# Optimization experiments

Hardware: AMD Instinct MI355X
Metric: run time of the kernel (lower is better)

Reference implementation:

```python
import jax, jax.numpy as jnp
import numpy as np

# ---- config constants (SmolLM2Config defaults) ----
N_EMBD = 576
N_HEAD = 9
N_KV = 3
HEAD_DIM = N_EMBD // N_HEAD        # 64
DR = 8                              # low-rank RoPE dim per head
GQA = N_HEAD // N_KV                # 9 // 3 = 3
BLOCK = 4096
ROPE_THETA = 100000.0
GROUP = 64                          # quant group size
RESID = 32                          # residual (full-precision) length
KBITS = 2
VBITS = 2
CLIP = 10000.0
B, S = 2, 2064


def _rope_tables():
    # pre_compute_rope with r=4 frequency indexing -> tables of width 2*r = 8 == DR
    pos = np.arange(BLOCK).astype(np.float32)
    thetas = 1.0 / ROPE_THETA ** (np.arange(0, HEAD_DIM, 2).astype(np.float32) / HEAD_DIM)
    pt = np.outer(pos, thetas)                       # [BLOCK, 32]
    pt = np.concatenate([pt, pt], axis=-1)           # [BLOCK, 64]
    cos, sin = np.cos(pt), np.sin(pt)
    r = 4
    idxs = sorted(sum([[2 * int(k * HEAD_DIM / (2 * r)), 2 * int(k * HEAD_DIM / (2 * r)) + 1]
                       for k in range(r)], []))      # [0,1,16,17,32,33,48,49]
    return jnp.asarray(cos[:, idxs]), jnp.asarray(sin[:, idxs])

COS, SIN = _rope_tables()  # each [BLOCK, DR]


def apply_rope(x):
    # x: [b, h, s, DR]; rotate-half RoPE on the DR low-rank dims
    s = x.shape[2]
    half = DR // 2
    x1, x2 = x[..., :half], x[..., half:]
    rotated = jnp.concatenate([-x2, x1], axis=-1)
    return x * COS[:s, :] + rotated * SIN[:s, :]


def _fake_quant(x, mn, mx, bits):
    levels = 2.0 ** bits - 1.0
    scale = (mx - mn) / levels
    scale = jnp.where(scale == 0, 1.0, scale)
    q = jnp.round((x - mn) / scale)
    return q * scale + mn


def quant_key(k):
    # AsymGroupedQuantizerByChannel: per-channel asym 2-bit over groups of GROUP tokens (STE)
    b, h, s, d = k.shape
    kf = jnp.clip(k, -CLIP, CLIP).reshape(b * h * (s // GROUP), GROUP, d)
    mn = kf.min(axis=1, keepdims=True)
    mx = kf.max(axis=1, keepdims=True)
    deq = _fake_quant(kf, mn, mx, KBITS)
    out = kf + jax.lax.stop_gradient(deq - kf)  # straight-through estimator
    return out.reshape(b, h, s, d)


def quant_value(v):
    # AsymGroupedQuantizer: per-token asym 2-bit over channel groups of size GROUP (== head_dim)
    b, h, s, d = v.shape
    vc = jnp.clip(v, -CLIP, CLIP)
    vg = vc.reshape(b, h, s, d // GROUP, GROUP)
    mn = vg.min(axis=-1, keepdims=True)
    mx = vg.max(axis=-1, keepdims=True)
    deq = _fake_quant(vg, mn, mx, VBITS).reshape(b, h, s, d)
    return vc + jax.lax.stop_gradient(deq - vc)


def maybe_quantize_kv(k, v):
    # KIVI: quantize all but the residual window
    s = k.shape[2]
    key_quant_len = (s // RESID) * RESID     # 2048 for S=2064
    value_quant_len = max(0, s - RESID)      # 2032
    k = jnp.concatenate([quant_key(k[:, :, :key_quant_len]), k[:, :, key_quant_len:]], axis=2)
    v = jnp.concatenate([quant_value(v[:, :, :value_quant_len]), v[:, :, value_quant_len:]], axis=2)
    return k, v


def setup_inputs() -> dict:
    key = jax.random.key(0)
    ks = jax.random.split(key, 7)
    std = 0.02
    return {
        "x": jax.random.normal(ks[0], (B, S, N_EMBD), jnp.float32),
        "q_w": jax.random.normal(ks[1], (N_HEAD * (HEAD_DIM - DR), N_EMBD), jnp.float32) * std,
        "k_w": jax.random.normal(ks[2], (N_KV * (HEAD_DIM - DR), N_EMBD), jnp.float32) * std,
        "v_w": jax.random.normal(ks[3], (N_KV * HEAD_DIM, N_EMBD), jnp.float32) * std,
        "qr_w": jax.random.normal(ks[4], (N_HEAD * DR, N_EMBD), jnp.float32) * std,
        "kr_w": jax.random.normal(ks[5], (N_KV * DR, N_EMBD), jnp.float32) * std,
        "o_w": jax.random.normal(ks[6], (N_EMBD, N_EMBD), jnp.float32) * std,
    }


def reference(x, q_w, k_w, v_w, qr_w, kr_w, o_w):
    b, s, _ = x.shape
    # projections (Linear: x @ W^T), split heads, [b, h, s, d]
    q = (x @ q_w.T).reshape(b, s, N_HEAD, HEAD_DIM - DR).transpose(0, 2, 1, 3)
    k = (x @ k_w.T).reshape(b, s, N_KV, HEAD_DIM - DR).transpose(0, 2, 1, 3)
    v = (x @ v_w.T).reshape(b, s, N_KV, HEAD_DIM).transpose(0, 2, 1, 3)
    qr = apply_rope((x @ qr_w.T).reshape(b, s, N_HEAD, DR).transpose(0, 2, 1, 3))
    kr = apply_rope((x @ kr_w.T).reshape(b, s, N_KV, DR).transpose(0, 2, 1, 3))
    q = jnp.concatenate([q, qr], axis=-1)   # [b, 9, s, 64]
    k = jnp.concatenate([k, kr], axis=-1)   # [b, 3, s, 64]
    # KIVI 2-bit fake-quantization of KV (residual window kept full precision)
    k, v = maybe_quantize_kv(k, v)
    # GQA: expand kv heads to query heads
    k = jnp.repeat(k, GQA, axis=1)
    v = jnp.repeat(v, GQA, axis=1)
    # causal attention
    scale = 1.0 / jnp.sqrt(jnp.float32(HEAD_DIM))
    scores = jnp.einsum('bhqd,bhkd->bhqk', q, k) * scale
    mask = jnp.tril(jnp.ones((s, s), bool))
    scores = jnp.where(mask, scores, -jnp.inf)
    attn = jax.nn.softmax(scores, axis=-1)
    out = jnp.einsum('bhqk,bhkd->bhqd', attn, v)
    out = out.transpose(0, 2, 1, 3).reshape(b, s, N_EMBD)
    return out @ o_w.T
```

## Files before the change

kernel.cpp:

```cpp
#include <hip/hip_runtime.h>
#include <math.h>

#define S_LEN 2064
#define S_PAD 2112
#define NB 2
#define NH 9
#define NKV 3
#define HD 64
#define EMB 576
#define NTOK (NB*S_LEN)
#define LSTR 68
#define KSTR 72

#define QSZ (NB*NH*S_LEN*HD)
#define KSZ (NB*NKV*S_LEN*HD)
#define VSZ (NB*NKV*S_LEN*HD)
#define ASZ (NB*S_LEN*EMB)
#define KPK (NB*NKV*S_PAD*HD)

#define NSLOT_BH 85
#define NSLOTS (NB*NH*NSLOT_BH)

typedef float  f32x4  __attribute__((ext_vector_type(4)));
typedef short  s16x8  __attribute__((ext_vector_type(8)));

static __device__ __forceinline__ ushort f2bf(float x) {
  union { float f; unsigned u; } a; a.f = x;
  unsigned r = a.u + 0x7fffu + ((a.u >> 16) & 1u);
  return (ushort)(r >> 16);
}
static __device__ __forceinline__ float bf2f(ushort h) {
  union { unsigned u; float f; } a; a.u = ((unsigned)h) << 16;
  return a.f;
}
static __device__ __forceinline__ int cum8(int qt) {
  int a = qt >> 3, b = qt & 7;
  return (a + 1) * (4 * a + b);
}

__global__ __launch_bounds__(256)
void proj_kernel(const float* __restrict__ x,
                 const float* __restrict__ qw, const float* __restrict__ kw,
                 const float* __restrict__ vw, const float* __restrict__ qrw,
                 const float* __restrict__ krw,
                 float* __restrict__ Qb, float* __restrict__ Kb,
                 float* __restrict__ Vb) {
  __shared__ __align__(16) ushort Xhi[64*KSTR];
  __shared__ __align__(16) ushort Xlo[64*KSTR];
  __shared__ __align__(16) ushort Whi[64*KSTR];
  __shared__ __align__(16) ushort Wlo[64*KSTR];

  const int tid  = threadIdx.x;
  const int wave = tid >> 6;
  const int lane = tid & 63;
  const int g    = lane >> 4;
  const int c    = lane & 15;

  const int m0 = blockIdx.x * 64;
  const int n0 = blockIdx.y * 64;

  const int srow = tid >> 2;
  const int sseg = (tid & 3) * 16;
  int gm = m0 + srow; if (gm > NTOK-1) gm = NTOK-1;
  const float* xrow = x + (size_t)gm * EMB;
  const int col = n0 + srow;
  const float* wrow;
  if (col < 504)      wrow = qw  + (size_t)col       * EMB;
  else if (col < 672) wrow = kw  + (size_t)(col-504) * EMB;
  else if (col < 864) wrow = vw  + (size_t)(col-672) * EMB;
  else if (col < 936) wrow = qrw + (size_t)(col-864) * EMB;
  else                wrow = krw + (size_t)(col-936) * EMB;

  f32x4 acc[4];
  #pragma unroll
  for (int n=0;n<4;++n) acc[n] = (f32x4){0.f,0.f,0.f,0.f};

  for (int kc0 = 0; kc0 < EMB; kc0 += 64) {
    __syncthreads();
    {
      float xv[16], wv[16];
      #pragma unroll
      for (int i=0;i<4;++i) {
        float4 x4 = *(const float4*)(xrow + kc0 + sseg + 4*i);
        float4 w4 = *(const float4*)(wrow + kc0 + sseg + 4*i);
        xv[4*i+0]=x4.x; xv[4*i+1]=x4.y; xv[4*i+2]=x4.z; xv[4*i+3]=x4.w;
        wv[4*i+0]=w4.x; wv[4*i+1]=w4.y; wv[4*i+2]=w4.z; wv[4*i+3]=w4.w;
      }
      uint xh[8], xl[8], wh[8], wl[8];
      #pragma unroll
      for (int m=0;m<8;++m) {
        ushort h0 = f2bf(xv[2*m]),   h1 = f2bf(xv[2*m+1]);
        ushort l0 = f2bf(xv[2*m]   - bf2f(h0));
        ushort l1 = f2bf(xv[2*m+1] - bf2f(h1));
        xh[m] = (uint)h0 | ((uint)h1 << 16);
        xl[m] = (uint)l0 | ((uint)l1 << 16);
        ushort g0 = f2bf(wv[2*m]),   g1 = f2bf(wv[2*m+1]);
        ushort k0 = f2bf(wv[2*m]   - bf2f(g0));
        ushort k1 = f2bf(wv[2*m+1] - bf2f(g1));
        wh[m] = (uint)g0 | ((uint)g1 << 16);
        wl[m] = (uint)k0 | ((uint)k1 << 16);
      }
      const int lo = srow*KSTR + sseg;
      *(uint4*)&Xhi[lo]     = make_uint4(xh[0],xh[1],xh[2],xh[3]);
      *(uint4*)&Xhi[lo + 8] = make_uint4(xh[4],xh[5],xh[6],xh[7]);
      *(uint4*)&Xlo[lo]     = make_uint4(xl[0],xl[1],xl[2],xl[3]);
      *(uint4*)&Xlo[lo + 8] = make_uint4(xl[4],xl[5],xl[6],xl[7]);
      *(uint4*)&Whi[lo]     = make_uint4(wh[0],wh[1],wh[2],wh[3]);
      *(uint4*)&Whi[lo + 8] = make_uint4(wh[4],wh[5],wh[6],wh[7]);
      *(uint4*)&Wlo[lo]     = make_uint4(wl[0],wl[1],wl[2],wl[3]);
      *(uint4*)&Wlo[lo + 8] = make_uint4(wl[4],wl[5],wl[6],wl[7]);
    }
    __syncthreads();

    #pragma unroll
    for (int kc=0; kc<2; ++kc) {
      const int d = kc*32 + g*8;
      s16x8 x_h = *(const s16x8*)&Xhi[(16*wave + c)*KSTR + d];
      s16x8 x_l = *(const s16x8*)&Xlo[(16*wave + c)*KSTR + d];
      #pragma unroll
      for (int n=0;n<4;++n) {
        s16x8 w_h = *(const s16x8*)&Whi[(16*n + c)*KSTR + d];
        s16x8 w_l = *(const s16x8*)&Wlo[(16*n + c)*KSTR + d];
        acc[n] = __builtin_amdgcn_mfma_f32_16x16x32_bf16(x_h, w_h, acc[n], 0, 0, 0);
        acc[n] = __builtin_amdgcn_mfma_f32_16x16x32_bf16(x_l, w_h, acc[n], 0, 0, 0);
        acc[n] = __builtin_amdgcn_mfma_f32_16x16x32_bf16(x_h, w_l, acc[n], 0, 0, 0);
        acc[n] = __builtin_amdgcn_mfma_f32_16x16x32_bf16(x_l, w_l, acc[n], 0, 0, 0);
      }
    }
  }

  #pragma unroll
  for (int r=0;r<4;++r) {
    const int row = m0 + 16*wave + 4*g + r;
    if (row >= NTOK) continue;
    const int b = row / S_LEN, s = row % S_LEN;
    #pragma unroll
    for (int n=0;n<4;++n) {
      const int cc = n0 + 16*n + c;
      const float v = acc[n][r];
      if (cc < 504) {
        int h = cc / 56, d = cc % 56;
        Qb[(((size_t)(b*NH+h))*S_LEN + s)*HD + d] = v;
      } else if (cc < 672) {
        int h = (cc-504)/56, d = (cc-504)%56;
        Kb[(((size_t)(b*NKV+h))*S_LEN + s)*HD + d] = v;
      } else if (cc < 864) {
        int h = (cc-672)/64, d = (cc-672)%64;
        Vb[(((size_t)(b*NKV+h))*S_LEN + s)*HD + d] = v;
      } else if (cc < 936) {
        int h = (cc-864)/8, d = 56 + (cc-864)%8;
        Qb[(((size_t)(b*NH+h))*S_LEN + s)*HD + d] = v;
      } else {
        int h = (cc-936)/8, d = 56 + (cc-936)%8;
        Kb[(((size_t)(b*NKV+h))*S_LEN + s)*HD + d] = v;
      }
    }
  }
}

__global__ void rope_kernel(float* __restrict__ Qb, float* __restrict__ Kb) {
  const int idx = blockIdx.x * blockDim.x + threadIdx.x;
  const int total = NB*(NH+NKV)*S_LEN;
  if (idx >= total) return;
  const int s  = idx % S_LEN;
  const int bh = idx / S_LEN;
  const int b  = bh / (NH+NKV), hh = bh % (NH+NKV);
  float* base;
  if (hh < NH) base = Qb + (((size_t)(b*NH + hh))*S_LEN + s)*HD + 56;
  else         base = Kb + (((size_t)(b*NKV + (hh-NH)))*S_LEN + s)*HD + 56;

  float4 a = *(const float4*)(base);
  float4 c = *(const float4*)(base + 4);
  float xv[8] = {a.x,a.y,a.z,a.w,c.x,c.y,c.z,c.w};
  const float es[4] = {0.0f, 2.0f/64.0f, 32.0f/64.0f, 34.0f/64.0f};
  const float ps = (float)s;
  float o[8];
  #pragma unroll
  for (int j=0;j<4;++j) {
    float th  = 1.0f / powf(100000.0f, es[j]);
    float ang = ps * th;
    float cs = cosf(ang), sn = sinf(ang);
    o[j]   = xv[j]*cs   - xv[j+4]*sn;
    o[j+4] = xv[j+4]*cs + xv[j]*sn;
  }
  *(float4*)(base)     = make_float4(o[0],o[1],o[2],o[3]);
  *(float4*)(base + 4) = make_float4(o[4],o[5],o[6],o[7]);
}

__global__ void quant_key_kernel(float* __restrict__ Kb) {
  const int wid  = (blockIdx.x * blockDim.x + threadIdx.x) >> 6;
  const int lane = threadIdx.x & 63;
  if (wid >= NB*NKV*32) return;
  const int bkh = wid >> 5, sg = wid & 31;
  float* base = Kb + ((size_t)bkh*S_LEN + sg*64)*HD + lane;
  float vals[64];
  float mn = 1e30f, mx = -1e30f;
  #pragma unroll
  for (int s=0;s<64;++s) {
    float v = fminf(fmaxf(base[s*HD], -10000.0f), 10000.0f);
    vals[s] = v;
    mn = fminf(mn, v); mx = fmaxf(mx, v);
  }
  float scale = (mx - mn) / 3.0f;
  if (scale == 0.0f) scale = 1.0f;
  #pragma unroll
  for (int s=0;s<64;++s) {
    float q = rintf((vals[s] - mn) / scale);
    base[s*HD] = q * scale + mn;
  }
}

__global__ void quant_value_kernel(float* __restrict__ Vb) {
  const int wid  = (blockIdx.x * blockDim.x + threadIdx.x) >> 6;
  const int lane = threadIdx.x & 63;
  const int total = NB*NKV*2032;
  if (wid >= total) return;
  const int bkh = wid / 2032, s = wid % 2032;
  float* p = Vb + ((size_t)bkh*S_LEN + s)*HD + lane;
  float v = fminf(fmaxf(*p, -10000.0f), 10000.0f);
  float mn = v, mx = v;
  #pragma unroll
  for (int m=1;m<64;m<<=1) {
    mn = fminf(mn, __shfl_xor(mn, m));
    mx = fmaxf(mx, __shfl_xor(mx, m));
  }
  float scale = (mx - mn) / 3.0f;
  if (scale == 0.0f) scale = 1.0f;
  float q = rintf((v - mn) / scale);
  *p = q * scale + mn;
}

__global__ __launch_bounds__(256)
void pack_k_kernel(const float* __restrict__ Kb,
                   ushort* __restrict__ KhiG, ushort* __restrict__ KloG) {
  const int idx = blockIdx.x * blockDim.x + threadIdx.x;
  const int total = NB*NKV*S_PAD*8;
  if (idx >= total) return;
  const int bkv = idx / (S_PAD*8);
  const int rem = idx % (S_PAD*8);
  const int s = rem >> 3, d0 = (rem & 7) * 8;
  uint u_h[4], u_l[4];
  if (s < S_LEN) {
    const float* src = Kb + ((size_t)bkv*S_LEN + s)*HD + d0;
    float4 a = *(const float4*)(src);
    float4 b = *(const float4*)(src + 4);
    float v[8] = {a.x,a.y,a.z,a.w,b.x,b.y,b.z,b.w};
    ushort hb[8], lb[8];
    #pragma unroll
    for (int e=0;e<8;++e) {
      hb[e] = f2bf(v[e]);
      lb[e] = f2bf(v[e] - bf2f(hb[e]));
    }
    #pragma unroll
    for (int m=0;m<4;++m) {
      u_h[m] = (uint)hb[2*m] | ((uint)hb[2*m+1] << 16);
      u_l[m] = (uint)lb[2*m] | ((uint)lb[2*m+1] << 16);
    }
  } else {
    #pragma unroll
    for (int m=0;m<4;++m) { u_h[m] = 0; u_l[m] = 0; }
  }
  const size_t off = ((size_t)bkv*S_PAD + s)*HD + d0;
  *(uint4*)(KhiG + off) = make_uint4(u_h[0],u_h[1],u_h[2],u_h[3]);
  *(uint4*)(KloG + off) = make_uint4(u_l[0],u_l[1],u_l[2],u_l[3]);
}

__global__ __launch_bounds__(256)
void pack_v_kernel(const float* __restrict__ Vb,
                   ushort* __restrict__ VhiT) {
  __shared__ float T[64*LSTR];
  const int tid = threadIdx.x;
  const int bkv = blockIdx.x / 33;
  const int kt  = blockIdx.x % 33;
  const int kbase = kt * 64;

  {
    const int key = tid >> 2, c16 = (tid & 3) * 16;
    const int s = kbase + key;
    if (s < S_LEN) {
      const float* src = Vb + ((size_t)bkv*S_LEN + s)*HD + c16;
      #pragma unroll
      for (int i=0;i<4;++i) {
        float4 v = *(const float4*)(src + 4*i);
        *(float4*)(T + key*LSTR + c16 + 4*i) = v;
      }
    } else {
      #pragma unroll
      for (int i=0;i<4;++i)
        *(float4*)(T + key*LSTR + c16 + 4*i) = make_float4(0.f,0.f,0.f,0.f);
    }
  }
  __syncthreads();
  {
    const int d = tid >> 2, seg = tid & 3;
    ushort hb[16];
    #pragma unroll
    for (int kk=0;kk<16;++kk)
      hb[kk] = f2bf(T[(seg*16 + kk)*LSTR + d]);
    uint uh[8];
    #pragma unroll
    for (int m=0;m<8;++m)
      uh[m] = (uint)hb[2*m] | ((uint)hb[2*m+1] << 16);
    const size_t off = ((size_t)bkv*HD + d)*S_PAD + kbase + seg*16;
    *(uint4*)(VhiT + off)     = make_uint4(uh[0],uh[1],uh[2],uh[3]);
    *(uint4*)(VhiT + off + 8) = make_uint4(uh[4],uh[5],uh[6],uh[7]);
  }
}

__global__ __launch_bounds__(256)
void attn_kernel(const float* __restrict__ Q,
                 const ushort* __restrict__ KhiG, const ushort* __restrict__ KloG,
                 const ushort* __restrict__ VhiT,
                 float* __restrict__ A,
                 float* __restrict__ Opart, float* __restrict__ Mpart,
                 float* __restrict__ Lpart, int CK) {
  __shared__ __align__(16) ushort Khi[64*KSTR];
  __shared__ __align__(16) ushort Klo[64*KSTR];
  __shared__ __align__(16) ushort Vhi[64*KSTR];
  __shared__ __align__(16) ushort Phi[64*KSTR];

  const int tid  = threadIdx.x;
  const int wave = tid >> 6;
  const int lane = tid & 63;
  const int g    = lane >> 4;
  const int c    = lane & 15;

  const int qt = 32 - (int)blockIdx.x;
  const int bh = blockIdx.y;
  const int ch = blockIdx.z;
  const int nch = (qt + CK) / CK;
  if (ch >= nch) return;
  const int kt0 = ch * CK;
  const int kt1 = min(kt0 + CK, qt + 1);

  const int b = bh / NH, h = bh % NH, kvh = h / (NH/NKV);
  const int bkv = b*NKV + kvh;
  const float* Qg = Q + ((size_t)(b*NH + h)*S_LEN)*HD;
  const ushort* KhiB = KhiG + (size_t)bkv*S_PAD*HD;
  const ushort* KloB = KloG + (size_t)bkv*S_PAD*HD;
  const ushort* VhiB = VhiT + (size_t)bkv*HD*S_PAD;
  const int qbase = qt * 64;

  s16x8 qhi[2], qlo[2];
  {
    int qrow = qbase + 16*wave + c;
    if (qrow > S_LEN-1) qrow = S_LEN-1;
    #pragma unroll
    for (int kc = 0; kc < 2; ++kc) {
      const float* qp = Qg + (size_t)qrow*HD + kc*32 + g*8;
      float4 q0 = *(const float4*)(qp);
      float4 q1 = *(const float4*)(qp + 4);
      float qv[8] = {q0.x,q0.y,q0.z,q0.w,q1.x,q1.y,q1.z,q1.w};
      #pragma unroll
      for (int e=0;e<8;++e) {
        ushort hi = f2bf(qv[e]);
        ushort lo = f2bf(qv[e] - bf2f(hi));
        qhi[kc][e] = (short)hi;
        qlo[kc][e] = (short)lo;
      }
    }
  }

  f32x4 acc_o[4];
  #pragma unroll
  for (int n=0;n<4;++n) acc_o[n] = (f32x4){0.f,0.f,0.f,0.f};
  float m_i[4], l_i[4];
  #pragma unroll
  for (int r=0;r<4;++r) { m_i[r] = -INFINITY; l_i[r] = 0.f; }

  const int srow = tid >> 3;
  const int sseg = (tid & 7) * 8;

  for (int kt = kt0; kt < kt1; ++kt) {
    const int kbase = kt * 64;
    __syncthreads();

    #pragma unroll
    for (int it=0; it<2; ++it) {
      const int r = srow + 32*it;
      const size_t kg = ((size_t)(kbase + r))*HD + sseg;
      *(uint4*)&Khi[r*KSTR + sseg] = *(const uint4*)(KhiB + kg);
      *(uint4*)&Klo[r*KSTR + sseg] = *(const uint4*)(KloB + kg);
      const size_t vg = (size_t)r*S_PAD + kbase + sseg;
      *(uint4*)&Vhi[r*KSTR + sseg] = *(const uint4*)(VhiB + vg);
    }
    __syncthreads();

    f32x4 sc[4];
    #pragma unroll
    for (int n=0;n<4;++n) sc[n] = (f32x4){0.f,0.f,0.f,0.f};
    #pragma unroll
    for (int kc=0; kc<2; ++kc) {
      #pragma unroll
      for (int n=0;n<4;++n) {
        const int key = 16*n + c;
        const int d   = kc*32 + g*8;
        s16x8 khf = *(const s16x8*)&Khi[key*KSTR + d];
        s16x8 klf = *(const s16x8*)&Klo[key*KSTR + d];
        sc[n] = __builtin_amdgcn_mfma_f32_16x16x32_bf16(qhi[kc], khf, sc[n], 0, 0, 0);
        sc[n] = __builtin_amdgcn_mfma_f32_16x16x32_bf16(qlo[kc], khf, sc[n], 0, 0, 0);
        sc[n] = __builtin_amdgcn_mfma_f32_16x16x32_bf16(qhi[kc], klf, sc[n], 0, 0, 0);
      }
    }

    const bool diag = (kt == qt);
    #pragma unroll
    for (int r=0;r<4;++r) {
      const int grow = qbase + 16*wave + 4*g + r;
      float s[4];
      #pragma unroll
      for (int n=0;n<4;++n) {
        float sv = sc[n][r] * 0.125f;
        if (diag && (kbase + 16*n + c > grow)) sv = -INFINITY;
        s[n] = sv;
      }
      float rm = fmaxf(fmaxf(s[0],s[1]), fmaxf(s[2],s[3]));
      rm = fmaxf(rm, __shfl_xor(rm, 1));
      rm = fmaxf(rm, __shfl_xor(rm, 2));
      rm = fmaxf(rm, __shfl_xor(rm, 4));
      rm = fmaxf(rm, __shfl_xor(rm, 8));
      const float mn = fmaxf(m_i[r], rm);
      const float al = __expf(m_i[r] - mn);
      float sum = 0.f;
      float pv4[4];
      #pragma unroll
      for (int n=0;n<4;++n) {
        float pv = __expf(s[n] - mn);
        pv4[n] = pv;
        sum += pv;
      }
      sum += __shfl_xor(sum, 1);
      sum += __shfl_xor(sum, 2);
      sum += __shfl_xor(sum, 4);
      sum += __shfl_xor(sum, 8);
      l_i[r] = l_i[r]*al + sum;
      m_i[r] = mn;
      #pragma unroll
      for (int n=0;n<4;++n) acc_o[n][r] *= al;
      #pragma unroll
      for (int n=0;n<4;++n)
        Phi[(16*wave + 4*g + r)*KSTR + 16*n + c] = f2bf(pv4[n]);
    }

    #pragma unroll
    for (int kc=0; kc<2; ++kc) {
      const int pd = kc*32 + g*8;
      s16x8 pfh = *(const s16x8*)&Phi[(16*wave + c)*KSTR + pd];
      #pragma unroll
      for (int n=0;n<4;++n) {
        s16x8 vfh = *(const s16x8*)&Vhi[(16*n + c)*KSTR + pd];
        acc_o[n] = __builtin_amdgcn_mfma_f32_16x16x32_bf16(pfh, vfh, acc_o[n], 0, 0, 0);
      }
    }
  }

  if (nch == 1) {
    #pragma unroll
    for (int r=0;r<4;++r) {
      const int grow = qbase + 16*wave + 4*g + r;
      if (grow < S_LEN) {
        const float inv = 1.0f / l_i[r];
        #pragma unroll
        for (int n=0;n<4;++n)
          A[((size_t)(b*S_LEN + grow))*EMB + h*HD + 16*n + c] = acc_o[n][r] * inv;
      }
    }
  } else {
    const int slot = bh*NSLOT_BH + cum8(qt) + ch;
    float* Ob = Opart + (size_t)slot * 4096;
    #pragma unroll
    for (int r=0;r<4;++r) {
      const int row = 16*wave + 4*g + r;
      #pragma unroll
      for (int n=0;n<4;++n)
        Ob[row*64 + 16*n + c] = acc_o[n][r];
      if (c == 0) {
        Mpart[(size_t)slot*64 + row] = m_i[r];
        Lpart[(size_t)slot*64 + row] = l_i[r];
      }
    }
  }
}

__global__ __launch_bounds__(256)
void attn_reduce_kernel(const float* __restrict__ Opart,
                        const float* __restrict__ Mpart,
                        const float* __restrict__ Lpart,
                        float* __restrict__ A) {
  const int qt = 8 + (int)blockIdx.x;
  const int bh = blockIdx.y;
  const int b = bh / NH, h = bh % NH;
  const int nch = (qt + 8) / 8;
  const int base = bh*NSLOT_BH + cum8(qt);

  const int tid = threadIdx.x;
  const int row = tid >> 2;
  const int seg = (tid & 3) * 16;
  const int grow = qt*64 + row;
  if (grow >= S_LEN) return;

  float mv[5], lv[5];
  float M = -INFINITY;
  for (int ch=0; ch<nch; ++ch) {
    mv[ch] = Mpart[(size_t)(base+ch)*64 + row];
    lv[ch] = Lpart[(size_t)(base+ch)*64 + row];
    M = fmaxf(M, mv[ch]);
  }
  float L = 0.f;
  float w[5];
  for (int ch=0; ch<nch; ++ch) {
    w[ch] = __expf(mv[ch] - M);
    L += lv[ch] * w[ch];
  }
  float o[16];
  #pragma unroll
  for (int j=0;j<16;++j) o[j] = 0.f;
  for (int ch=0; ch<nch; ++ch) {
    const float* Ob = Opart + (size_t)(base+ch)*4096 + row*64 + seg;
    const float wc = w[ch];
    #pragma unroll
    for (int i=0;i<4;++i) {
      float4 v = *(const float4*)(Ob + 4*i);
      o[4*i+0] += wc*v.x; o[4*i+1] += wc*v.y;
      o[4*i+2] += wc*v.z; o[4*i+3] += wc*v.w;
    }
  }
  const float inv = 1.0f / L;
  float* dst = A + ((size_t)(b*S_LEN + grow))*EMB + h*HD + seg;
  #pragma unroll
  for (int i=0;i<4;++i)
    *(float4*)(dst + 4*i) = make_float4(o[4*i]*inv, o[4*i+1]*inv,
                                        o[4*i+2]*inv, o[4*i+3]*inv);
}

__global__ __launch_bounds__(256)
void oproj_kernel(const float* __restrict__ A, const float* __restrict__ ow,
                  float* __restrict__ out) {
  __shared__ __align__(16) ushort Ahi[64*KSTR];
  __shared__ __align__(16) ushort Alo[64*KSTR];
  __shared__ __align__(16) ushort Whi[64*KSTR];
  __shared__ __align__(16) ushort Wlo[64*KSTR];

  const int tid  = threadIdx.x;
  const int wave = tid >> 6;
  const int lane = tid & 63;
  const int g    = lane >> 4;
  const int c    = lane & 15;

  const int m0 = blockIdx.x * 64;
  const int n0 = blockIdx.y * 64;

  const int srow = tid >> 2;
  const int sseg = (tid & 3) * 16;
  int am = m0 + srow; if (am > NTOK-1) am = NTOK-1;
  const float* arow = A  + (size_t)am * EMB;
  const float* wrow = ow + (size_t)(n0 + srow) * EMB;

  f32x4 acc[4];
  #pragma unroll
  for (int n=0;n<4;++n) acc[n] = (f32x4){0.f,0.f,0.f,0.f};

  for (int kc0 = 0; kc0 < EMB; kc0 += 64) {
    __syncthreads();
    {
      float av[16], wv[16];
      #pragma unroll
      for (int i=0;i<4;++i) {
        float4 a4 = *(const float4*)(arow + kc0 + sseg + 4*i);
        float4 w4 = *(const float4*)(wrow + kc0 + sseg + 4*i);
        av[4*i+0]=a4.x; av[4*i+1]=a4.y; av[4*i+2]=a4.z; av[4*i+3]=a4.w;
        wv[4*i+0]=w4.x; wv[4*i+1]=w4.y; wv[4*i+2]=w4.z; wv[4*i+3]=w4.w;
      }
      uint ah[8], al[8], wh[8], wl[8];
      #pragma unroll
      for (int m=0;m<8;++m) {
        ushort h0 = f2bf(av[2*m]),   h1 = f2bf(av[2*m+1]);
        ushort l0 = f2bf(av[2*m]   - bf2f(h0));
        ushort l1 = f2bf(av[2*m+1] - bf2f(h1));
        ah[m] = (uint)h0 | ((uint)h1 << 16);
        al[m] = (uint)l0 | ((uint)l1 << 16);
        ushort g0 = f2bf(wv[2*m]),   g1 = f2bf(wv[2*m+1]);
        ushort m0_ = f2bf(wv[2*m]   - bf2f(g0));
        ushort m1_ = f2bf(wv[2*m+1] - bf2f(g1));
        wh[m] = (uint)g0 | ((uint)g1 << 16);
        wl[m] = (uint)m0_ | ((uint)m1_ << 16);
      }
      const int lo = srow*KSTR + sseg;
      *(uint4*)&Ahi[lo]     = make_uint4(ah[0],ah[1],ah[2],ah[3]);
      *(uint4*)&Ahi[lo + 8] = make_uint4(ah[4],ah[5],ah[6],ah[7]);
      *(uint4*)&Alo[lo]     = make_uint4(al[0],al[1],al[2],al[3]);
      *(uint4*)&Alo[lo + 8] = make_uint4(al[4],al[5],al[6],al[7]);
      *(uint4*)&Whi[lo]     = make_uint4(wh[0],wh[1],wh[2],wh[3]);
      *(uint4*)&Whi[lo + 8] = make_uint4(wh[4],wh[5],wh[6],wh[7]);
      *(uint4*)&Wlo[lo]     = make_uint4(wl[0],wl[1],wl[2],wl[3]);
      *(uint4*)&Wlo[lo + 8] = make_uint4(wl[4],wl[5],wl[6],wl[7]);
    }
    __syncthreads();

    #pragma unroll
    for (int kc=0; kc<2; ++kc) {
      const int d = kc*32 + g*8;
      s16x8 a_h = *(const s16x8*)&Ahi[(16*wave + c)*KSTR + d];
      s16x8 a_l = *(const s16x8*)&Alo[(16*wave + c)*KSTR + d];
      #pragma unroll
      for (int n=0;n<4;++n) {
        s16x8 w_h = *(const s16x8*)&Whi[(16*n + c)*KSTR + d];
        s16x8 w_l = *(const s16x8*)&Wlo[(16*n + c)*KSTR + d];
        acc[n] = __builtin_amdgcn_mfma_f32_16x16x32_bf16(a_h, w_h, acc[n], 0, 0, 0);
        acc[n] = __builtin_amdgcn_mfma_f32_16x16x32_bf16(a_l, w_h, acc[n], 0, 0, 0);
        acc[n] = __builtin_amdgcn_mfma_f32_16x16x32_bf16(a_h, w_l, acc[n], 0, 0, 0);
      }
    }
  }

  #pragma unroll
  for (int r=0;r<4;++r) {
    const int m = m0 + 16*wave + 4*g + r;
    if (m < NTOK) {
      #pragma unroll
      for (int n=0;n<4;++n)
        out[(size_t)m*EMB + n0 + 16*n + c] = acc[n][r];
    }
  }
}

extern "C" void kernel_launch(void* const* d_in, const int* in_sizes, int n_in,
                              void* d_out, int out_size, void* d_ws, size_t ws_size,
                              hipStream_t stream) {
  const float* x   = (const float*)d_in[0];
  const float* qw  = (const float*)d_in[1];
  const float* kw  = (const float*)d_in[2];
  const float* vw  = (const float*)d_in[3];
  const float* qrw = (const float*)d_in[4];
  const float* krw = (const float*)d_in[5];
  const float* ow  = (const float*)d_in[6];
  float* out = (float*)d_out;

  float* ws = (float*)d_ws;
  float* Qb = ws;
  float* Kb = Qb + QSZ;
  float* Vb = Kb + KSZ;
  float* Ab = Vb + VSZ;
  ushort* KhiG = (ushort*)(Ab + ASZ);
  ushort* KloG = KhiG + KPK;
  ushort* VhiT = KloG + KPK;
  float* Opart = (float*)(VhiT + KPK);
  float* Mpart = Opart + (size_t)NSLOTS*4096;
  float* Lpart = Mpart + (size_t)NSLOTS*64;

  const size_t need = (size_t)((char*)(Lpart + (size_t)NSLOTS*64) - (char*)d_ws);
  const bool splitk = (ws_size >= need);

  dim3 g1((NTOK + 63)/64, 960/64);
  proj_kernel<<<g1, 256, 0, stream>>>(x, qw, kw, vw, qrw, krw, Qb, Kb, Vb);

  {
    int total = NB*(NH+NKV)*S_LEN;
    rope_kernel<<<(total+255)/256, 256, 0, stream>>>(Qb, Kb);
  }

  {
    int kwaves = NB*NKV*32;
    quant_key_kernel<<<(kwaves*64+255)/256, 256, 0, stream>>>(Kb);
    int vwaves = NB*NKV*2032;
    quant_value_kernel<<<(vwaves*64+255)/256, 256, 0, stream>>>(Vb);
  }

  {
    int ksegs = NB*NKV*S_PAD*8;
    pack_k_kernel<<<(ksegs+255)/256, 256, 0, stream>>>(Kb, KhiG, KloG);
    pack_v_kernel<<<NB*NKV*33, 256, 0, stream>>>(Vb, VhiT);
  }

  if (splitk) {
    dim3 ga(33, NB*NH, 5);
    attn_kernel<<<ga, 256, 0, stream>>>(Qb, KhiG, KloG, VhiT, Ab,
                                        Opart, Mpart, Lpart, 8);
    dim3 gr(25, NB*NH);
    attn_reduce_kernel<<<gr, 256, 0, stream>>>(Opart, Mpart, Lpart, Ab);
  } else {
    dim3 ga(33, NB*NH, 1);
    attn_kernel<<<ga, 256, 0, stream>>>(Qb, KhiG, KloG, VhiT, Ab,
                                        Opart, Mpart, Lpart, 33);
  }

  dim3 go((NTOK + 63)/64, EMB/64);
  oproj_kernel<<<go, 256, 0, stream>>>(Ab, ow, out);
}
```

Baseline: 220.4 us.

## Pre-split inputs to bf16 hi/lo once and fuse KV quantization into packing

A new pack kernel converts x and all weights to bf16 hi/lo pairs once, so the projection GEMM loads ready-made bf16 tiles instead of re-splitting fp32 in every block. The attention output is written directly as bf16 hi/lo for the output projection. K and V fake-quantization now happens inside the pack kernels, removing two launches and one read/write pass over K and V. The split-K slot layout is compacted, and the packed buffers alias the Opart workspace. The trade-off is an extra launch plus extra memory traffic to write the pre-split arrays.

```diff
diff --git a/kernel.cpp b/kernel.cpp
--- a/kernel.cpp
+++ b/kernel.cpp
@@ -17,8 +17,10 @@
 #define VSZ (NB*NKV*S_LEN*HD)
 #define ASZ (NB*S_LEN*EMB)
 #define KPK (NB*NKV*S_PAD*HD)
-
-#define NSLOT_BH 85
+#define WCAT (960*EMB)
+#define OWSZ (EMB*EMB)
+
+#define NSLOT_BH 77
 #define NSLOTS (NB*NH*NSLOT_BH)
 
 typedef float  f32x4  __attribute__((ext_vector_type(4)));
@@ -37,12 +39,71 @@
   int a = qt >> 3, b = qt & 7;
   return (a + 1) * (4 * a + b);
 }
-
+static __device__ __forceinline__ void split8(const float* v, uint* uh, uint* ul) {
+  ushort hb[8], lb[8];
+  #pragma unroll
+  for (int e=0;e<8;++e) {
+    hb[e] = f2bf(v[e]);
+    lb[e] = f2bf(v[e] - bf2f(hb[e]));
+  }
+  #pragma unroll
+  for (int m=0;m<4;++m) {
+    uh[m] = (uint)hb[2*m] | ((uint)hb[2*m+1] << 16);
+    ul[m] = (uint)lb[2*m] | ((uint)lb[2*m+1] << 16);
+  }
+}
+
+#define XSEG (NTOK*72)
+#define WSEG (960*72)
+#define OSEG (EMB*72)
 __global__ __launch_bounds__(256)
-void proj_kernel(const float* __restrict__ x,
-                 const float* __restrict__ qw, const float* __restrict__ kw,
-                 const float* __restrict__ vw, const float* __restrict__ qrw,
-                 const float* __restrict__ krw,
+void pack_inputs_kernel(const float* __restrict__ x,
+                        const float* __restrict__ qw, const float* __restrict__ kw,
+                        const float* __restrict__ vw, const float* __restrict__ qrw,
+                        const float* __restrict__ krw, const float* __restrict__ ow,
+                        ushort* __restrict__ XhiG, ushort* __restrict__ XloG,
+                        ushort* __restrict__ WcatHi, ushort* __restrict__ WcatLo,
+                        ushort* __restrict__ OWhi, ushort* __restrict__ OWlo) {
+  const int idx = blockIdx.x * blockDim.x + threadIdx.x;
+  if (idx >= XSEG + WSEG + OSEG) return;
+  const float* src;
+  ushort *dh, *dl;
+  if (idx < XSEG) {
+    const int row = idx / 72, seg = (idx % 72) * 8;
+    src = x + (size_t)row*EMB + seg;
+    dh = XhiG + (size_t)row*EMB + seg;
+    dl = XloG + (size_t)row*EMB + seg;
+  } else if (idx < XSEG + WSEG) {
+    const int j = idx - XSEG;
+    const int col = j / 72, seg = (j % 72) * 8;
+    const float* wrow;
+    if (col < 504)      wrow = qw  + (size_t)col       * EMB;
+    else if (col < 672) wrow = kw  + (size_t)(col-504) * EMB;
+    else if (col < 864) wrow = vw  + (size_t)(col-672) * EMB;
+    else if (col < 936) wrow = qrw + (size_t)(col-864) * EMB;
+    else                wrow = krw + (size_t)(col-936) * EMB;
+    src = wrow + seg;
+    dh = WcatHi + (size_t)col*EMB + seg;
+    dl = WcatLo + (size_t)col*EMB + seg;
+  } else {
+    const int j = idx - XSEG - WSEG;
+    const int row = j / 72, seg = (j % 72) * 8;
+    src = ow + (size_t)row*EMB + seg;
+    dh = OWhi + (size_t)row*EMB + seg;
+    dl = OWlo + (size_t)row*EMB + seg;
+  }
+  float4 a = *(const float4*)(src);
+  float4 b = *(const float4*)(src + 4);
+  float v[8] = {a.x,a.y,a.z,a.w,b.x,b.y,b.z,b.w};
+  uint uh[4], ul[4];
+  split8(v, uh, ul);
+  *(uint4*)dh = make_uint4(uh[0],uh[1],uh[2],uh[3]);
+  *(uint4*)dl = make_uint4(ul[0],ul[1],ul[2],ul[3]);
+}
+
+__global__ __launch_bounds__(256)
+void proj_kernel(const ushort* __restrict__ XhiG, const ushort* __restrict__ XloG,
+                 const ushort* __restrict__ WcatHi, const ushort* __restrict__ WcatLo,
                  float* __restrict__ Qb, float* __restrict__ Kb,
                  float* __restrict__ Vb) {
   __shared__ __align__(16) ushort Xhi[64*KSTR];
@@ -62,14 +123,10 @@
   const int srow = tid >> 2;
   const int sseg = (tid & 3) * 16;
   int gm = m0 + srow; if (gm > NTOK-1) gm = NTOK-1;
-  const float* xrow = x + (size_t)gm * EMB;
-  const int col = n0 + srow;
-  const float* wrow;
-  if (col < 504)      wrow = qw  + (size_t)col       * EMB;
-  else if (col < 672) wrow = kw  + (size_t)(col-504) * EMB;
-  else if (col < 864) wrow = vw  + (size_t)(col-672) * EMB;
-  else if (col < 936) wrow = qrw + (size_t)(col-864) * EMB;
-  else                wrow = krw + (size_t)(col-936) * EMB;
+  const ushort* xh = XhiG + (size_t)gm*EMB;
+  const ushort* xl = XloG + (size_t)gm*EMB;
+  const ushort* wh = WcatHi + (size_t)(n0 + srow)*EMB;
+  const ushort* wl = WcatLo + (size_t)(n0 + srow)*EMB;
 
   f32x4 acc[4];
   #pragma unroll
@@ -78,37 +135,16 @@
   for (int kc0 = 0; kc0 < EMB; kc0 += 64) {
     __syncthreads();
     {
-      float xv[16], wv[16];
-      #pragma unroll
-      for (int i=0;i<4;++i) {
-        float4 x4 = *(const float4*)(xrow + kc0 + sseg + 4*i);
-        float4 w4 = *(const float4*)(wrow + kc0 + sseg + 4*i);
-        xv[4*i+0]=x4.x; xv[4*i+1]=x4.y; xv[4*i+2]=x4.z; xv[4*i+3]=x4.w;
-        wv[4*i+0]=w4.x; wv[4*i+1]=w4.y; wv[4*i+2]=w4.z; wv[4*i+3]=w4.w;
-      }
-      uint xh[8], xl[8], wh[8], wl[8];
-      #pragma unroll
-      for (int m=0;m<8;++m) {
-        ushort h0 = f2bf(xv[2*m]),   h1 = f2bf(xv[2*m+1]);
-        ushort l0 = f2bf(xv[2*m]   - bf2f(h0));
-        ushort l1 = f2bf(xv[2*m+1] - bf2f(h1));
-        xh[m] = (uint)h0 | ((uint)h1 << 16);
-        xl[m] = (uint)l0 | ((uint)l1 << 16);
-        ushort g0 = f2bf(wv[2*m]),   g1 = f2bf(wv[2*m+1]);
-        ushort k0 = f2bf(wv[2*m]   - bf2f(g0));
-        ushort k1 = f2bf(wv[2*m+1] - bf2f(g1));
-        wh[m] = (uint)g0 | ((uint)g1 << 16);
-        wl[m] = (uint)k0 | ((uint)k1 << 16);
-      }
+      const int go = kc0 + sseg;
       const int lo = srow*KSTR + sseg;
-      *(uint4*)&Xhi[lo]     = make_uint4(xh[0],xh[1],xh[2],xh[3]);
-      *(uint4*)&Xhi[lo + 8] = make_uint4(xh[4],xh[5],xh[6],xh[7]);
-      *(uint4*)&Xlo[lo]     = make_uint4(xl[0],xl[1],xl[2],xl[3]);
-      *(uint4*)&Xlo[lo + 8] = make_uint4(xl[4],xl[5],xl[6],xl[7]);
-      *(uint4*)&Whi[lo]     = make_uint4(wh[0],wh[1],wh[2],wh[3]);
-      *(uint4*)&Whi[lo + 8] = make_uint4(wh[4],wh[5],wh[6],wh[7]);
-      *(uint4*)&Wlo[lo]     = make_uint4(wl[0],wl[1],wl[2],wl[3]);
-      *(uint4*)&Wlo[lo + 8] = make_uint4(wl[4],wl[5],wl[6],wl[7]);
+      *(uint4*)&Xhi[lo]     = *(const uint4*)(xh + go);
+      *(uint4*)&Xhi[lo + 8] = *(const uint4*)(xh + go + 8);
+      *(uint4*)&Xlo[lo]     = *(const uint4*)(xl + go);
+      *(uint4*)&Xlo[lo + 8] = *(const uint4*)(xl + go + 8);
+      *(uint4*)&Whi[lo]     = *(const uint4*)(wh + go);
+      *(uint4*)&Whi[lo + 8] = *(const uint4*)(wh + go + 8);
+      *(uint4*)&Wlo[lo]     = *(const uint4*)(wl + go);
+      *(uint4*)&Wlo[lo + 8] = *(const uint4*)(wl + go + 8);
     }
     __syncthreads();
 
@@ -187,116 +223,137 @@
   *(float4*)(base + 4) = make_float4(o[4],o[5],o[6],o[7]);
 }
 
-__global__ void quant_key_kernel(float* __restrict__ Kb) {
-  const int wid  = (blockIdx.x * blockDim.x + threadIdx.x) >> 6;
-  const int lane = threadIdx.x & 63;
-  if (wid >= NB*NKV*32) return;
-  const int bkh = wid >> 5, sg = wid & 31;
-  float* base = Kb + ((size_t)bkh*S_LEN + sg*64)*HD + lane;
-  float vals[64];
-  float mn = 1e30f, mx = -1e30f;
-  #pragma unroll
-  for (int s=0;s<64;++s) {
-    float v = fminf(fmaxf(base[s*HD], -10000.0f), 10000.0f);
-    vals[s] = v;
-    mn = fminf(mn, v); mx = fmaxf(mx, v);
-  }
-  float scale = (mx - mn) / 3.0f;
-  if (scale == 0.0f) scale = 1.0f;
-  #pragma unroll
-  for (int s=0;s<64;++s) {
-    float q = rintf((vals[s] - mn) / scale);
-    base[s*HD] = q * scale + mn;
-  }
-}
-
-__global__ void quant_value_kernel(float* __restrict__ Vb) {
-  const int wid  = (blockIdx.x * blockDim.x + threadIdx.x) >> 6;
-  const int lane = threadIdx.x & 63;
-  const int total = NB*NKV*2032;
-  if (wid >= total) return;
-  const int bkh = wid / 2032, s = wid % 2032;
-  float* p = Vb + ((size_t)bkh*S_LEN + s)*HD + lane;
-  float v = fminf(fmaxf(*p, -10000.0f), 10000.0f);
-  float mn = v, mx = v;
-  #pragma unroll
-  for (int m=1;m<64;m<<=1) {
-    mn = fminf(mn, __shfl_xor(mn, m));
-    mx = fmaxf(mx, __shfl_xor(mx, m));
-  }
-  float scale = (mx - mn) / 3.0f;
-  if (scale == 0.0f) scale = 1.0f;
-  float q = rintf((v - mn) / scale);
-  *p = q * scale + mn;
-}
-
 __global__ __launch_bounds__(256)
-void pack_k_kernel(const float* __restrict__ Kb,
+void packqk_kernel(const float* __restrict__ Kb,
                    ushort* __restrict__ KhiG, ushort* __restrict__ KloG) {
-  const int idx = blockIdx.x * blockDim.x + threadIdx.x;
-  const int total = NB*NKV*S_PAD*8;
-  if (idx >= total) return;
-  const int bkv = idx / (S_PAD*8);
-  const int rem = idx % (S_PAD*8);
-  const int s = rem >> 3, d0 = (rem & 7) * 8;
-  uint u_h[4], u_l[4];
-  if (s < S_LEN) {
-    const float* src = Kb + ((size_t)bkv*S_LEN + s)*HD + d0;
-    float4 a = *(const float4*)(src);
-    float4 b = *(const float4*)(src + 4);
-    float v[8] = {a.x,a.y,a.z,a.w,b.x,b.y,b.z,b.w};
-    ushort hb[8], lb[8];
-    #pragma unroll
-    for (int e=0;e<8;++e) {
-      hb[e] = f2bf(v[e]);
-      lb[e] = f2bf(v[e] - bf2f(hb[e]));
-    }
-    #pragma unroll
-    for (int m=0;m<4;++m) {
-      u_h[m] = (uint)hb[2*m] | ((uint)hb[2*m+1] << 16);
-      u_l[m] = (uint)lb[2*m] | ((uint)lb[2*m+1] << 16);
-    }
-  } else {
-    #pragma unroll
-    for (int m=0;m<4;++m) { u_h[m] = 0; u_l[m] = 0; }
-  }
-  const size_t off = ((size_t)bkv*S_PAD + s)*HD + d0;
-  *(uint4*)(KhiG + off) = make_uint4(u_h[0],u_h[1],u_h[2],u_h[3]);
-  *(uint4*)(KloG + off) = make_uint4(u_l[0],u_l[1],u_l[2],u_l[3]);
-}
-
-__global__ __launch_bounds__(256)
-void pack_v_kernel(const float* __restrict__ Vb,
-                   ushort* __restrict__ VhiT) {
   __shared__ float T[64*LSTR];
+  __shared__ float PMN[4][64], PMX[4][64];
+  __shared__ float MN[64], SC[64];
   const int tid = threadIdx.x;
   const int bkv = blockIdx.x / 33;
   const int kt  = blockIdx.x % 33;
   const int kbase = kt * 64;
 
   {
-    const int key = tid >> 2, c16 = (tid & 3) * 16;
-    const int s = kbase + key;
+    const int r = tid >> 2, c16 = (tid & 3) * 16;
+    const int s = kbase + r;
+    if (s < S_LEN) {
+      const float* src = Kb + ((size_t)bkv*S_LEN + s)*HD + c16;
+      #pragma unroll
+      for (int i=0;i<4;++i)
+        *(float4*)(T + r*LSTR + c16 + 4*i) = *(const float4*)(src + 4*i);
+    } else {
+      #pragma unroll
+      for (int i=0;i<4;++i)
+        *(float4*)(T + r*LSTR + c16 + 4*i) = make_float4(0.f,0.f,0.f,0.f);
+    }
+  }
+  __syncthreads();
+
+  if (kt < 32) {
+    const int d = tid & 63, q = tid >> 6;
+    float mn = 1e30f, mx = -1e30f;
+    #pragma unroll
+    for (int i=0;i<16;++i) {
+      float v = fminf(fmaxf(T[(16*q + i)*LSTR + d], -10000.0f), 10000.0f);
+      mn = fminf(mn, v); mx = fmaxf(mx, v);
+    }
+    PMN[q][d] = mn; PMX[q][d] = mx;
+    __syncthreads();
+    if (tid < 64) {
+      float m0 = fminf(fminf(PMN[0][tid],PMN[1][tid]), fminf(PMN[2][tid],PMN[3][tid]));
+      float m1 = fmaxf(fmaxf(PMX[0][tid],PMX[1][tid]), fmaxf(PMX[2][tid],PMX[3][tid]));
+      float sc = (m1 - m0) / 3.0f;
+      if (sc == 0.0f) sc = 1.0f;
+      MN[tid] = m0; SC[tid] = sc;
+    }
+    __syncthreads();
+  }
+
+  {
+    const int r = tid >> 2, c16 = (tid & 3) * 16;
+    float v16[16];
+    #pragma unroll
+    for (int j=0;j<16;++j) {
+      const int d = c16 + j;
+      float v = T[r*LSTR + d];
+      if (kt < 32) {
+        v = fminf(fmaxf(v, -10000.0f), 10000.0f);
+        v = rintf((v - MN[d]) / SC[d]) * SC[d] + MN[d];
+      }
+      v16[j] = v;
+    }
+    uint uh[8], ul[8];
+    split8(v16,     uh,     ul);
+    split8(v16 + 8, uh + 4, ul + 4);
+    const size_t off = ((size_t)bkv*S_PAD + kbase + r)*HD + c16;
+    *(uint4*)(KhiG + off)     = make_uint4(uh[0],uh[1],uh[2],uh[3]);
+    *(uint4*)(KhiG + off + 8) = make_uint4(uh[4],uh[5],uh[6],uh[7]);
+    *(uint4*)(KloG + off)     = make_uint4(ul[0],ul[1],ul[2],ul[3]);
+    *(uint4*)(KloG + off + 8) = make_uint4(ul[4],ul[5],ul[6],ul[7]);
+  }
+}
+
+__global__ __launch_bounds__(256)
+void packqv_kernel(const float* __restrict__ Vb,
+                   ushort* __restrict__ VhiT) {
+  __shared__ float T[64*LSTR];
+  __shared__ float PMN[4][64], PMX[4][64];
+  __shared__ float MN[64], SC[64];
+  const int tid = threadIdx.x;
+  const int bkv = blockIdx.x / 33;
+  const int kt  = blockIdx.x % 33;
+  const int kbase = kt * 64;
+
+  {
+    const int r = tid >> 2, c16 = (tid & 3) * 16;
+    const int s = kbase + r;
     if (s < S_LEN) {
       const float* src = Vb + ((size_t)bkv*S_LEN + s)*HD + c16;
       #pragma unroll
-      for (int i=0;i<4;++i) {
-        float4 v = *(const float4*)(src + 4*i);
-        *(float4*)(T + key*LSTR + c16 + 4*i) = v;
-      }
+      for (int i=0;i<4;++i)
+        *(float4*)(T + r*LSTR + c16 + 4*i) = *(const float4*)(src + 4*i);
     } else {
       #pragma unroll
       for (int i=0;i<4;++i)
-        *(float4*)(T + key*LSTR + c16 + 4*i) = make_float4(0.f,0.f,0.f,0.f);
+        *(float4*)(T + r*LSTR + c16 + 4*i) = make_float4(0.f,0.f,0.f,0.f);
     }
   }
   __syncthreads();
+
+  {
+    const int r = tid & 63, q = tid >> 6;
+    float mn = 1e30f, mx = -1e30f;
+    #pragma unroll
+    for (int i=0;i<16;++i) {
+      float v = fminf(fmaxf(T[r*LSTR + 16*q + i], -10000.0f), 10000.0f);
+      mn = fminf(mn, v); mx = fmaxf(mx, v);
+    }
+    PMN[q][r] = mn; PMX[q][r] = mx;
+  }
+  __syncthreads();
+  if (tid < 64) {
+    float m0 = fminf(fminf(PMN[0][tid],PMN[1][tid]), fminf(PMN[2][tid],PMN[3][tid]));
+    float m1 = fmaxf(fmaxf(PMX[0][tid],PMX[1][tid]), fmaxf(PMX[2][tid],PMX[3][tid]));
+    float sc = (m1 - m0) / 3.0f;
+    if (sc == 0.0f) sc = 1.0f;
+    MN[tid] = m0; SC[tid] = sc;
+  }
+  __syncthreads();
+
   {
     const int d = tid >> 2, seg = tid & 3;
     ushort hb[16];
     #pragma unroll
-    for (int kk=0;kk<16;++kk)
-      hb[kk] = f2bf(T[(seg*16 + kk)*LSTR + d]);
+    for (int j=0;j<16;++j) {
+      const int k = 16*seg + j;
+      float v = T[k*LSTR + d];
+      if (kbase + k < 2032) {
+        v = fminf(fmaxf(v, -10000.0f), 10000.0f);
+        v = rintf((v - MN[k]) / SC[k]) * SC[k] + MN[k];
+      }
+      hb[j] = f2bf(v);
+    }
     uint uh[8];
     #pragma unroll
     for (int m=0;m<8;++m)
@@ -311,7 +368,7 @@
 void attn_kernel(const float* __restrict__ Q,
                  const ushort* __restrict__ KhiG, const ushort* __restrict__ KloG,
                  const ushort* __restrict__ VhiT,
-                 float* __restrict__ A,
+                 ushort* __restrict__ AhiG, ushort* __restrict__ AloG,
                  float* __restrict__ Opart, float* __restrict__ Mpart,
                  float* __restrict__ Lpart, int CK) {
   __shared__ __align__(16) ushort Khi[64*KSTR];
@@ -460,13 +517,18 @@
       const int grow = qbase + 16*wave + 4*g + r;
       if (grow < S_LEN) {
         const float inv = 1.0f / l_i[r];
+        const size_t base = ((size_t)(b*S_LEN + grow))*EMB + h*HD;
         #pragma unroll
-        for (int n=0;n<4;++n)
-          A[((size_t)(b*S_LEN + grow))*EMB + h*HD + 16*n + c] = acc_o[n][r] * inv;
+        for (int n=0;n<4;++n) {
+          float v = acc_o[n][r] * inv;
+          ushort hh = f2bf(v);
+          AhiG[base + 16*n + c] = hh;
+          AloG[base + 16*n + c] = f2bf(v - bf2f(hh));
+        }
       }
     }
   } else {
-    const int slot = bh*NSLOT_BH + cum8(qt) + ch;
+    const int slot = bh*NSLOT_BH + (cum8(qt) - 8) + ch;
     float* Ob = Opart + (size_t)slot * 4096;
     #pragma unroll
     for (int r=0;r<4;++r) {
@@ -486,12 +548,12 @@
 void attn_reduce_kernel(const float* __restrict__ Opart,
                         const float* __restrict__ Mpart,
                         const float* __restrict__ Lpart,
-                        float* __restrict__ A) {
+                        ushort* __restrict__ AhiG, ushort* __restrict__ AloG) {
   const int qt = 8 + (int)blockIdx.x;
   const int bh = blockIdx.y;
   const int b = bh / NH, h = bh % NH;
   const int nch = (qt + 8) / 8;
-  const int base = bh*NSLOT_BH + cum8(qt);
+  const int base = bh*NSLOT_BH + (cum8(qt) - 8);
 
   const int tid = threadIdx.x;
   const int row = tid >> 2;
@@ -526,15 +588,22 @@
     }
   }
   const float inv = 1.0f / L;
-  float* dst = A + ((size_t)(b*S_LEN + grow))*EMB + h*HD + seg;
-  #pragma unroll
-  for (int i=0;i<4;++i)
-    *(float4*)(dst + 4*i) = make_float4(o[4*i]*inv, o[4*i+1]*inv,
-                                        o[4*i+2]*inv, o[4*i+3]*inv);
+  float v16[16];
+  #pragma unroll
+  for (int j=0;j<16;++j) v16[j] = o[j]*inv;
+  uint uh[8], ul[8];
+  split8(v16,     uh,     ul);
+  split8(v16 + 8, uh + 4, ul + 4);
+  const size_t dst = ((size_t)(b*S_LEN + grow))*EMB + h*HD + seg;
+  *(uint4*)(AhiG + dst)     = make_uint4(uh[0],uh[1],uh[2],uh[3]);
+  *(uint4*)(AhiG + dst + 8) = make_uint4(uh[4],uh[5],uh[6],uh[7]);
+  *(uint4*)(AloG + dst)     = make_uint4(ul[0],ul[1],ul[2],ul[3]);
+  *(uint4*)(AloG + dst + 8) = make_uint4(ul[4],ul[5],ul[6],ul[7]);
 }
 
 __global__ __launch_bounds__(256)
-void oproj_kernel(const float* __restrict__ A, const float* __restrict__ ow,
+void oproj_kernel(const ushort* __restrict__ AhiG, const ushort* __restrict__ AloG,
+                  const ushort* __restrict__ OWhi, const ushort* __restrict__ OWlo,
                   float* __restrict__ out) {
   __shared__ __align__(16) ushort Ahi[64*KSTR];
   __shared__ __align__(16) ushort Alo[64*KSTR];
@@ -553,8 +622,10 @@
   const int srow = tid >> 2;
   const int sseg = (tid & 3) * 16;
   int am = m0 + srow; if (am > NTOK-1) am = NTOK-1;
-  const float* arow = A  + (size_t)am * EMB;
-  const float* wrow = ow + (size_t)(n0 + srow) * EMB;
+  const ushort* ah = AhiG + (size_t)am*EMB;
+  const ushort* al = AloG + (size_t)am*EMB;
+  const ushort* wh = OWhi + (size_t)(n0 + srow)*EMB;
+  const ushort* wl = OWlo + (size_t)(n0 + srow)*EMB;
 
   f32x4 acc[4];
   #pragma unroll
@@ -563,37 +634,16 @@
   for (int kc0 = 0; kc0 < EMB; kc0 += 64) {
     __syncthreads();
     {
-      float av[16], wv[16];
-      #pragma unroll
-      for (int i=0;i<4;++i) {
-        float4 a4 = *(const float4*)(arow + kc0 + sseg + 4*i);
-        float4 w4 = *(const float4*)(wrow + kc0 + sseg + 4*i);
-        av[4*i+0]=a4.x; av[4*i+1]=a4.y; av[4*i+2]=a4.z; av[4*i+3]=a4.w;
-        wv[4*i+0]=w4.x; wv[4*i+1]=w4.y; wv[4*i+2]=w4.z; wv[4*i+3]=w4.w;
-      }
-      uint ah[8], al[8], wh[8], wl[8];
-      #pragma unroll
-      for (int m=0;m<8;++m) {
-        ushort h0 = f2bf(av[2*m]),   h1 = f2bf(av[2*m+1]);
-        ushort l0 = f2bf(av[2*m]   - bf2f(h0));
-        ushort l1 = f2bf(av[2*m+1] - bf2f(h1));
-        ah[m] = (uint)h0 | ((uint)h1 << 16);
-        al[m] = (uint)l0 | ((uint)l1 << 16);
-        ushort g0 = f2bf(wv[2*m]),   g1 = f2bf(wv[2*m+1]);
-        ushort m0_ = f2bf(wv[2*m]   - bf2f(g0));
-        ushort m1_ = f2bf(wv[2*m+1] - bf2f(g1));
-        wh[m] = (uint)g0 | ((uint)g1 << 16);
-        wl[m] = (uint)m0_ | ((uint)m1_ << 16);
-      }
+      const int go = kc0 + sseg;
       const int lo = srow*KSTR + sseg;
-      *(uint4*)&Ahi[lo]     = make_uint4(ah[0],ah[1],ah[2],ah[3]);
-      *(uint4*)&Ahi[lo + 8] = make_uint4(ah[4],ah[5],ah[6],ah[7]);
-      *(uint4*)&Alo[lo]     = make_uint4(al[0],al[1],al[2],al[3]);
-      *(uint4*)&Alo[lo + 8] = make_uint4(al[4],al[5],al[6],al[7]);
-      *(uint4*)&Whi[lo]     = make_uint4(wh[0],wh[1],wh[2],wh[3]);
-      *(uint4*)&Whi[lo + 8] = make_uint4(wh[4],wh[5],wh[6],wh[7]);
-      *(uint4*)&Wlo[lo]     = make_uint4(wl[0],wl[1],wl[2],wl[3]);
-      *(uint4*)&Wlo[lo + 8] = make_uint4(wl[4],wl[5],wl[6],wl[7]);
+      *(uint4*)&Ahi[lo]     = *(const uint4*)(ah + go);
+      *(uint4*)&Ahi[lo + 8] = *(const uint4*)(ah + go + 8);
+      *(uint4*)&Alo[lo]     = *(const uint4*)(al + go);
+      *(uint4*)&Alo[lo + 8] = *(const uint4*)(al + go + 8);
+      *(uint4*)&Whi[lo]     = *(const uint4*)(wh + go);
+      *(uint4*)&Whi[lo + 8] = *(const uint4*)(wh + go + 8);
+      *(uint4*)&Wlo[lo]     = *(const uint4*)(wl + go);
+      *(uint4*)&Wlo[lo + 8] = *(const uint4*)(wl + go + 8);
     }
     __syncthreads();
 
@@ -640,50 +690,53 @@
   float* Qb = ws;
   float* Kb = Qb + QSZ;
   float* Vb = Kb + KSZ;
-  float* Ab = Vb + VSZ;
-  ushort* KhiG = (ushort*)(Ab + ASZ);
+  ushort* KhiG = (ushort*)(Vb + VSZ);
   ushort* KloG = KhiG + KPK;
   ushort* VhiT = KloG + KPK;
-  float* Opart = (float*)(VhiT + KPK);
-  float* Mpart = Opart + (size_t)NSLOTS*4096;
+  ushort* AhiG = VhiT + KPK;
+  ushort* AloG = AhiG + ASZ;
+  ushort* OWhi = AloG + ASZ;
+  ushort* OWlo = OWhi + OWSZ;
+  float* Mpart = (float*)(OWlo + OWSZ);
   float* Lpart = Mpart + (size_t)NSLOTS*64;
-
-  const size_t need = (size_t)((char*)(Lpart + (size_t)NSLOTS*64) - (char*)d_ws);
+  float* Opart = Lpart + (size_t)NSLOTS*64;
+  ushort* XhiG   = (ushort*)Opart;
+  ushort* XloG   = XhiG + (size_t)NTOK*EMB;
+  ushort* WcatHi = XloG + (size_t)NTOK*EMB;
+  ushort* WcatLo = WcatHi + WCAT;
+
+  const size_t need = (size_t)((char*)(Opart + (size_t)NSLOTS*4096) - (char*)d_ws);
   const bool splitk = (ws_size >= need);
 
+  {
+    int total = XSEG + WSEG + OSEG;
+    pack_inputs_kernel<<<(total+255)/256, 256, 0, stream>>>(
+        x, qw, kw, vw, qrw, krw, ow, XhiG, XloG, WcatHi, WcatLo, OWhi, OWlo);
+  }
+
   dim3 g1((NTOK + 63)/64, 960/64);
-  proj_kernel<<<g1, 256, 0, stream>>>(x, qw, kw, vw, qrw, krw, Qb, Kb, Vb);
+  proj_kernel<<<g1, 256, 0, stream>>>(XhiG, XloG, WcatHi, WcatLo, Qb, Kb, Vb);
 
   {
     int total = NB*(NH+NKV)*S_LEN;
     rope_kernel<<<(total+255)/256, 256, 0, stream>>>(Qb, Kb);
   }
 
-  {
-    int kwaves = NB*NKV*32;
-    quant_key_kernel<<<(kwaves*64+255)/256, 256, 0, stream>>>(Kb);
-    int vwaves = NB*NKV*2032;
-    quant_value_kernel<<<(vwaves*64+255)/256, 256, 0, stream>>>(Vb);
-  }
-
-  {
-    int ksegs = NB*NKV*S_PAD*8;
-    pack_k_kernel<<<(ksegs+255)/256, 256, 0, stream>>>(Kb, KhiG, KloG);
-    pack_v_kernel<<<NB*NKV*33, 256, 0, stream>>>(Vb, VhiT);
-  }
+  packqk_kernel<<<NB*NKV*33, 256, 0, stream>>>(Kb, KhiG, KloG);
+  packqv_kernel<<<NB*NKV*33, 256, 0, stream>>>(Vb, VhiT);
 
   if (splitk) {
     dim3 ga(33, NB*NH, 5);
-    attn_kernel<<<ga, 256, 0, stream>>>(Qb, KhiG, KloG, VhiT, Ab,
+    attn_kernel<<<ga, 256, 0, stream>>>(Qb, KhiG, KloG, VhiT, AhiG, AloG,
                                         Opart, Mpart, Lpart, 8);
     dim3 gr(25, NB*NH);
-    attn_reduce_kernel<<<gr, 256, 0, stream>>>(Opart, Mpart, Lpart, Ab);
+    attn_reduce_kernel<<<gr, 256, 0, stream>>>(Opart, Mpart, Lpart, AhiG, AloG);
   } else {
     dim3 ga(33, NB*NH, 1);
-    attn_kernel<<<ga, 256, 0, stream>>>(Qb, KhiG, KloG, VhiT, Ab,
+    attn_kernel<<<ga, 256, 0, stream>>>(Qb, KhiG, KloG, VhiT, AhiG, AloG,
                                         Opart, Mpart, Lpart, 33);
   }
 
   dim3 go((NTOK + 63)/64, EMB/64);
-  oproj_kernel<<<go, 256, 0, stream>>>(Ab, ow, out);
-}
+  oproj_kernel<<<go, 256, 0, stream>>>(AhiG, AloG, OWhi, OWlo, out);
+}
```

Measured after the change: 211.2 us. 4.2% less time.
